# Optimization experiments

Hardware: AMD Instinct MI355X
Metric: run time of the kernel (lower is better)

## Reference

```python
import jax, jax.numpy as jnp
import numpy as np

N = 65536      # total nodes = B * MAXN
E = 524288     # edges (avg degree 8)
DX = 32; DG = 32
IN_DIM = DX + 3 * DG   # 128, after concat(x, g0, g1, g2)
H = 256; OUT = 8; MAXN = 8192


def setup_inputs() -> dict:
    key = jax.random.key(0)
    ks = jax.random.split(key, 40)
    inp = {}
    inp['x'] = jax.random.normal(ks[0], (N, DX), jnp.float32)
    inp['g0'] = jax.random.normal(ks[1], (N, DG), jnp.float32)
    inp['g1'] = jax.random.normal(ks[2], (N, DG), jnp.float32)
    inp['g2'] = jax.random.normal(ks[3], (N, DG), jnp.float32)
    inp['edge_src'] = jax.random.randint(ks[4], (E,), 0, N, jnp.int32)
    inp['edge_dst'] = jax.random.randint(ks[5], (E,), 0, N, jnp.int32)
    dims = [(IN_DIM, H), (H, H), (H, H), (H, H)]
    k = 6
    for i, (di, do) in enumerate(dims):
        s = 1.0 / np.sqrt(di)
        inp[f'Wl{i}'] = jax.random.uniform(ks[k], (di, do), jnp.float32, -s, s); k += 1
        inp[f'Wr{i}'] = jax.random.uniform(ks[k], (di, do), jnp.float32, -s, s); k += 1
        inp[f'b{i}'] = jnp.zeros((do,), jnp.float32)
    s = 1.0 / np.sqrt(MAXN)
    inp['mlp1_W1'] = jax.random.uniform(ks[k], (MAXN, H), jnp.float32, -s, s); k += 1
    inp['mlp1_b1'] = jnp.zeros((H,), jnp.float32)
    s = 1.0 / np.sqrt(H)
    inp['mlp1_W2'] = jax.random.uniform(ks[k], (H, 1), jnp.float32, -s, s); k += 1
    inp['mlp1_b2'] = jnp.zeros((1,), jnp.float32)
    inp['bn_gamma'] = jnp.ones((H,), jnp.float32)
    inp['bn_beta'] = jnp.zeros((H,), jnp.float32)
    inp['mlp2_W1'] = jax.random.uniform(ks[k], (H, H), jnp.float32, -s, s); k += 1
    inp['mlp2_b1'] = jnp.zeros((H,), jnp.float32)
    inp['mlp2_W2'] = jax.random.uniform(ks[k], (H, OUT), jnp.float32, -s, s); k += 1
    inp['mlp2_b2'] = jnp.zeros((OUT,), jnp.float32)
    return inp


def _forward(x, g0, g1, g2, edge_src, edge_dst,
             Wl0, Wr0, b0, Wl1, Wr1, b1, Wl2, Wr2, b2, Wl3, Wr3, b3,
             mlp1_W1, mlp1_b1, mlp1_W2, mlp1_b2, bn_gamma, bn_beta,
             mlp2_W1, mlp2_b1, mlp2_W2, mlp2_b2):
    h = jnp.concatenate([x, g0, g1, g2], axis=1)  # [N, IN_DIM]
    # mean-aggregation denominator (in-degree, clamped at 1 like PyG mean)
    cnt = jnp.maximum(
        jax.ops.segment_sum(jnp.ones((E,), h.dtype), edge_dst, num_segments=N), 1.0)
    for Wl, Wr, b in ((Wl0, Wr0, b0), (Wl1, Wr1, b1), (Wl2, Wr2, b2), (Wl3, Wr3, b3)):
        agg = jax.ops.segment_sum(h[edge_src], edge_dst, num_segments=N) / cnt[:, None]
        # SAGEConv: lin_l(mean of neighbors) + lin_r(self) + bias, then ReLU
        h = jax.nn.relu(agg @ Wl + h @ Wr + b)
        # F.dropout in eval / deterministic reference: identity
    h = h.reshape(-1, H, MAXN)                               # [B, H, MAXN]
    h = jax.nn.relu(jnp.einsum('bhm,mk->bhk', h, mlp1_W1) + mlp1_b1)
    h = (jnp.einsum('bhk,ko->bho', h, mlp1_W2) + mlp1_b2)[..., 0]  # [B, H]
    mean = h.mean(axis=0)
    var = h.var(axis=0)
    h = (h - mean) / jnp.sqrt(var + 1e-5) * bn_gamma + bn_beta
    h = jax.nn.relu(h)
    h = jax.nn.relu(h @ mlp2_W1 + mlp2_b1)
    return h @ mlp2_W2 + mlp2_b2                              # [B, OUT]


def reference(x, g0, g1, g2, edge_src, edge_dst,
              Wl0, Wr0, b0, Wl1, Wr1, b1, Wl2, Wr2, b2, Wl3, Wr3, b3,
              mlp1_W1, mlp1_b1, mlp1_W2, mlp1_b2, bn_gamma, bn_beta,
              mlp2_W1, mlp2_b1, mlp2_W2, mlp2_b2):
    return _forward(x, g0, g1, g2, edge_src, edge_dst,
                    Wl0, Wr0, b0, Wl1, Wr1, b1, Wl2, Wr2, b2, Wl3, Wr3, b3,
                    mlp1_W1, mlp1_b1, mlp1_W2, mlp1_b2, bn_gamma, bn_beta,
                    mlp2_W1, mlp2_b1, mlp2_W2, mlp2_b2)
```

## Files before the change

kernel.cpp:

```cpp
#include <hip/hip_runtime.h>
#include <hip/hip_bf16.h>


#define NN 65536
#define EE 524288
#define ROWS 65537
#define PCSR_CAP 983056

using frag16 = __attribute__((ext_vector_type(8))) short;
using f32x4  = __attribute__((ext_vector_type(4))) float;

__device__ __forceinline__ float b2f(unsigned short u) {
    union { unsigned u32; float f; } x; x.u32 = (unsigned)u << 16; return x.f;
}

__device__ __forceinline__ unsigned short f2b(float f) {
    return (unsigned short)(__bfloat16_as_ushort(__float2bfloat16(f)));
}

__device__ __forceinline__ void gld_lds16(const void* g, void* l) {
    __builtin_amdgcn_global_load_lds(
        (const __attribute__((address_space(1))) void*)g,
        (__attribute__((address_space(3))) void*)l, 16, 0, 0);
}


__global__ void gs_zero_deg(int* deg) {
    int i = blockIdx.x * 256 + threadIdx.x;
    if (i < NN) deg[i] = 0;
}

__global__ void gs_hist(const int* __restrict__ dst, int* __restrict__ deg) {
    int e = blockIdx.x * 256 + threadIdx.x;
    atomicAdd(&deg[dst[e]], 1);
}

__global__ void gs_deg_reduce(const int* __restrict__ deg, int* __restrict__ bsum) {
    int t = threadIdx.x;
    int p = (deg[blockIdx.x * 256 + t] + 7) & ~7;
#pragma unroll
    for (int off = 32; off > 0; off >>= 1) p += __shfl_down(p, off);
    __shared__ int w4[4];
    if ((t & 63) == 0) w4[t >> 6] = p;
    __syncthreads();
    if (t == 0) bsum[blockIdx.x] = w4[0] + w4[1] + w4[2] + w4[3];
}

__global__ void gs_scan_bsum(const int* __restrict__ bsum, int* __restrict__ bofs,
                             int* __restrict__ prow) {
    __shared__ int part[256];
    int t = threadIdx.x;
    int v = bsum[t];
    part[t] = v;
    __syncthreads();
    for (int off = 1; off < 256; off <<= 1) {
        int add = (t >= off) ? part[t - off] : 0;
        __syncthreads();
        part[t] += add;
        __syncthreads();
    }
    bofs[t] = part[t] - v;
    if (t == 255) prow[NN] = part[255];
}

__global__ void gs_scan_apply(const int* __restrict__ deg, const int* __restrict__ bofs,
                              int* __restrict__ prow, int* __restrict__ cursor,
                              float* __restrict__ inv_cnt, int* __restrict__ pcsr,
                              __hip_bfloat16* __restrict__ P0,
                              __hip_bfloat16* __restrict__ P1) {
    __shared__ int part[256];
    int t = threadIdx.x;
    int i = blockIdx.x * 256 + t;
    int d = deg[i];
    int p = (d + 7) & ~7;
    part[t] = p;
    __syncthreads();
    for (int off = 1; off < 256; off <<= 1) {
        int add = (t >= off) ? part[t - off] : 0;
        __syncthreads();
        part[t] += add;
        __syncthreads();
    }
    int beg = bofs[blockIdx.x] + part[t] - p;
    prow[i] = beg;
    cursor[i] = beg;
    inv_cnt[i] = 1.0f / (float)(d > 0 ? d : 1);
    for (int j = d; j < p; ++j) pcsr[beg + j] = NN;
    if (blockIdx.x == 0) {
        ((unsigned*)(P0 + (size_t)NN * 512))[t] = 0u;
        ((unsigned*)(P1 + (size_t)NN * 512))[t] = 0u;
        if (t < 16) pcsr[PCSR_CAP - 16 + t] = NN;
    }
}

__global__ void gs_bucket(const int* __restrict__ src, const int* __restrict__ dst,
                          int* __restrict__ cursor, int* __restrict__ pcsr) {
    int e = blockIdx.x * 256 + threadIdx.x;
    int d = dst[e];
    int p = atomicAdd(&cursor[d], 1);
    pcsr[p] = src[e];
}

struct TcvtArgs {
    const float* src[8];
    __hip_bfloat16* dst[8];
    int ldk[8];
    int kofs[8];
    int kblk[8];
};

__global__ void gs_tcvt_all(TcvtArgs a) {
    int z = blockIdx.z;
    if ((int)blockIdx.x >= a.kblk[z]) return;
    const float* src = a.src[z];
    __hip_bfloat16* dst = a.dst[z];
    int ldk = a.ldk[z], kofs = a.kofs[z];
    __shared__ float tile[32][33];
    int kb = blockIdx.x * 32, nb = blockIdx.y * 32;
    int tx = threadIdx.x, ty = threadIdx.y;
#pragma unroll
    for (int i = 0; i < 32; i += 8)
        tile[ty + i][tx] = src[(size_t)(kb + ty + i) * 256 + nb + tx];
    __syncthreads();
#pragma unroll
    for (int i = 0; i < 32; i += 8) {
        int n = nb + ty + i, k = kb + tx;
        dst[(size_t)n * ldk + kofs + k] = __float2bfloat16(tile[tx][ty + i]);
    }
}

__global__ void gs_tcvt(const float* __restrict__ src, __hip_bfloat16* __restrict__ dst,
                        int ldk, int kofs) {
    __shared__ float tile[32][33];
    int kb = blockIdx.x * 32, nb = blockIdx.y * 32;
    int tx = threadIdx.x, ty = threadIdx.y;
#pragma unroll
    for (int i = 0; i < 32; i += 8)
        tile[ty + i][tx] = src[(size_t)(kb + ty + i) * 256 + nb + tx];
    __syncthreads();
#pragma unroll
    for (int i = 0; i < 32; i += 8) {
        int n = nb + ty + i, k = kb + tx;
        dst[(size_t)n * ldk + kofs + k] = __float2bfloat16(tile[tx][ty + i]);
    }
}

__global__ void gs_concat_bf(const float* __restrict__ x, const float* __restrict__ g0,
                             const float* __restrict__ g1, const float* __restrict__ g2,
                             __hip_bfloat16* __restrict__ h) {
    int idx = blockIdx.x * 256 + threadIdx.x;
    int n = idx >> 7, c = idx & 127;
    float v;
    if (c < 32)       v = x[n * 32 + c];
    else if (c < 64)  v = g0[n * 32 + (c - 32)];
    else if (c < 96)  v = g1[n * 32 + (c - 64)];
    else              v = g2[n * 32 + (c - 96)];
    h[(size_t)n * 512 + 256 + c] = __float2bfloat16(v);
}

template <int DIM>
__global__ void gs_agg_bf(const __hip_bfloat16* __restrict__ hsrc,
                          __hip_bfloat16* __restrict__ adst,
                          const int* __restrict__ prow, const int* __restrict__ pcsr,
                          const float* __restrict__ inv_cnt) {
    int wave = threadIdx.x >> 6;
    int lane = threadIdx.x & 63;
    int n = blockIdx.x * 4 + wave;
    int e = prow[n], pe = prow[n + 1];
    float iv = inv_cnt[n];
    if constexpr (DIM == 256) {
        const __hip_bfloat16* base = hsrc + lane * 4;
        float a0 = 0.f, a1 = 0.f, a2 = 0.f, a3 = 0.f;
        int4 ia = *(const int4*)(pcsr + e);
        int4 ib = *(const int4*)(pcsr + e + 4);
        while (e < pe) {
            int4 c0 = ia, c1 = ib;
            e += 8;
            ia = *(const int4*)(pcsr + e);
            ib = *(const int4*)(pcsr + e + 4);
            ushort4 v0 = *(const ushort4*)(base + (size_t)c0.x * 512);
            ushort4 v1 = *(const ushort4*)(base + (size_t)c0.y * 512);
            ushort4 v2 = *(const ushort4*)(base + (size_t)c0.z * 512);
            ushort4 v3 = *(const ushort4*)(base + (size_t)c0.w * 512);
            ushort4 v4 = *(const ushort4*)(base + (size_t)c1.x * 512);
            ushort4 v5 = *(const ushort4*)(base + (size_t)c1.y * 512);
            ushort4 v6 = *(const ushort4*)(base + (size_t)c1.z * 512);
            ushort4 v7 = *(const ushort4*)(base + (size_t)c1.w * 512);
            a0 += b2f(v0.x); a1 += b2f(v0.y); a2 += b2f(v0.z); a3 += b2f(v0.w);
            a0 += b2f(v1.x); a1 += b2f(v1.y); a2 += b2f(v1.z); a3 += b2f(v1.w);
            a0 += b2f(v2.x); a1 += b2f(v2.y); a2 += b2f(v2.z); a3 += b2f(v2.w);
            a0 += b2f(v3.x); a1 += b2f(v3.y); a2 += b2f(v3.z); a3 += b2f(v3.w);
            a0 += b2f(v4.x); a1 += b2f(v4.y); a2 += b2f(v4.z); a3 += b2f(v4.w);
            a0 += b2f(v5.x); a1 += b2f(v5.y); a2 += b2f(v5.z); a3 += b2f(v5.w);
            a0 += b2f(v6.x); a1 += b2f(v6.y); a2 += b2f(v6.z); a3 += b2f(v6.w);
            a0 += b2f(v7.x); a1 += b2f(v7.y); a2 += b2f(v7.z); a3 += b2f(v7.w);
        }
        __hip_bfloat16 o[4] = {__float2bfloat16(a0 * iv), __float2bfloat16(a1 * iv),
                               __float2bfloat16(a2 * iv), __float2bfloat16(a3 * iv)};
        *(ushort4*)(adst + (size_t)n * 512 + lane * 4) = *(const ushort4*)o;
    } else {
        const __hip_bfloat16* base = hsrc + lane * 2;
        float a0 = 0.f, a1 = 0.f;
        int4 ia = *(const int4*)(pcsr + e);
        int4 ib = *(const int4*)(pcsr + e + 4);
        while (e < pe) {
            int4 c0 = ia, c1 = ib;
            e += 8;
            ia = *(const int4*)(pcsr + e);
            ib = *(const int4*)(pcsr + e + 4);
            ushort2 v0 = *(const ushort2*)(base + (size_t)c0.x * 512);
            ushort2 v1 = *(const ushort2*)(base + (size_t)c0.y * 512);
            ushort2 v2 = *(const ushort2*)(base + (size_t)c0.z * 512);
            ushort2 v3 = *(const ushort2*)(base + (size_t)c0.w * 512);
            ushort2 v4 = *(const ushort2*)(base + (size_t)c1.x * 512);
            ushort2 v5 = *(const ushort2*)(base + (size_t)c1.y * 512);
            ushort2 v6 = *(const ushort2*)(base + (size_t)c1.z * 512);
            ushort2 v7 = *(const ushort2*)(base + (size_t)c1.w * 512);
            a0 += b2f(v0.x); a1 += b2f(v0.y);
            a0 += b2f(v1.x); a1 += b2f(v1.y);
            a0 += b2f(v2.x); a1 += b2f(v2.y);
            a0 += b2f(v3.x); a1 += b2f(v3.y);
            a0 += b2f(v4.x); a1 += b2f(v4.y);
            a0 += b2f(v5.x); a1 += b2f(v5.y);
            a0 += b2f(v6.x); a1 += b2f(v6.y);
            a0 += b2f(v7.x); a1 += b2f(v7.y);
        }
        __hip_bfloat16 o[2] = {__float2bfloat16(a0 * iv), __float2bfloat16(a1 * iv)};
        *(ushort2*)(adst + (size_t)n * 512 + lane * 2) = *(const ushort2*)o;
    }
}

__device__ __forceinline__ void mfma_block_n256(const __hip_bfloat16* A, int lda,
                                                const __hip_bfloat16* Bt, int ldb,
                                                int kbeg, int kend, size_t row0,
                                                __hip_bfloat16* As, __hip_bfloat16* Bs,
                                                f32x4 acc[4][8]) {
    const int t = threadIdx.x;
    const int lane = t & 63;
    const int w = t >> 6;
    const int wr = (w >> 1) * 64;
    const int wc = (w & 1) * 128;
    const int sr8 = lane >> 3;
    const int scol = (lane & 7) * 8;
    for (int kc = kbeg; kc < kend; kc += 64) {
#pragma unroll
        for (int l = 0; l < 4; ++l)
            gld_lds16(A + (row0 + w * 32 + 8 * l + sr8) * (size_t)lda + kc + scol,
                      As + (w * 32 + 8 * l) * 64);
#pragma unroll
        for (int l = 0; l < 8; ++l)
            gld_lds16(Bt + (size_t)(w * 64 + 8 * l + sr8) * ldb + kc + scol,
                      Bs + (w * 64 + 8 * l) * 64);
        __syncthreads();
#pragma unroll
        for (int kk = 0; kk < 64; kk += 32) {
            frag16 af[4];
#pragma unroll
            for (int i = 0; i < 4; ++i)
                af[i] = *(const frag16*)(As + (wr + i * 16 + (lane & 15)) * 64 + kk + (lane >> 4) * 8);
#pragma unroll
            for (int j = 0; j < 8; ++j) {
                frag16 bf = *(const frag16*)(Bs + (wc + j * 16 + (lane & 15)) * 64 + kk + (lane >> 4) * 8);
#pragma unroll
                for (int i = 0; i < 4; ++i)
                    acc[i][j] = __builtin_amdgcn_mfma_f32_16x16x32_bf16(bf, af[i], acc[i][j], 0, 0, 0);
            }
        }
        __syncthreads();
    }
}

__global__ __launch_bounds__(256, 2)
void gs_gemm_bias_relu(const __hip_bfloat16* __restrict__ A, int lda, int K,
                       const __hip_bfloat16* __restrict__ Bt, int ldb,
                       const float* __restrict__ bias,
                       __hip_bfloat16* __restrict__ C, int ldc, int cofs) {
    __shared__ __hip_bfloat16 As[128 * 64];
    __shared__ __hip_bfloat16 Bs[256 * 64];
    f32x4 acc[4][8] = {};
    const size_t row0 = (size_t)blockIdx.x * 128;
    mfma_block_n256(A, lda, Bt, ldb, 0, K, row0, As, Bs, acc);
    const int lane = threadIdx.x & 63;
    const int w = threadIdx.x >> 6;
    const int wr = (w >> 1) * 64, wc = (w & 1) * 128;
#pragma unroll
    for (int j = 0; j < 8; ++j) {
        int nb = wc + j * 16 + (lane >> 4) * 4;
        const float4 bv = *(const float4*)&bias[nb];
#pragma unroll
        for (int i = 0; i < 4; ++i) {
            int m = wr + i * 16 + (lane & 15);
            unsigned short o[4];
            o[0] = f2b(fmaxf(acc[i][j][0] + bv.x, 0.f));
            o[1] = f2b(fmaxf(acc[i][j][1] + bv.y, 0.f));
            o[2] = f2b(fmaxf(acc[i][j][2] + bv.z, 0.f));
            o[3] = f2b(fmaxf(acc[i][j][3] + bv.w, 0.f));
            *(ushort4*)(C + (row0 + m) * (size_t)ldc + cofs + nb) = *(const ushort4*)o;
        }
    }
}

__global__ __launch_bounds__(256, 2)
void gs_gemm_splitk(const __hip_bfloat16* __restrict__ A, int lda,
                    const __hip_bfloat16* __restrict__ Bt, int ldb,
                    float* __restrict__ part) {
    __shared__ __hip_bfloat16 As[128 * 64];
    __shared__ __hip_bfloat16 Bs[256 * 64];
    f32x4 acc[4][8] = {};
    const size_t row0 = (size_t)blockIdx.x * 128;
    const int kbeg = blockIdx.y * 512;
    mfma_block_n256(A, lda, Bt, ldb, kbeg, kbeg + 512, row0, As, Bs, acc);
    const int lane = threadIdx.x & 63;
    const int w = threadIdx.x >> 6;
    const int wr = (w >> 1) * 64, wc = (w & 1) * 128;
    float* p = part + (size_t)blockIdx.y * 2048 * 256;
#pragma unroll
    for (int j = 0; j < 8; ++j) {
        int nb = wc + j * 16 + (lane >> 4) * 4;
#pragma unroll
        for (int i = 0; i < 4; ++i) {
            int m = wr + i * 16 + (lane & 15);
            *(f32x4*)(p + (row0 + m) * 256 + nb) = acc[i][j];
        }
    }
}

__global__ void gs_mlp1_reduce_pool(const float* __restrict__ part,
                                    const float* __restrict__ b1,
                                    const float* __restrict__ W2,
                                    const float* __restrict__ b2,
                                    float* __restrict__ pooled) {
    __shared__ float w4[4];
    int r = blockIdx.x;
    int t = threadIdx.x;
    size_t idx = (size_t)r * 256 + t;
    float s = 0.f;
#pragma unroll
    for (int ks = 0; ks < 16; ++ks) s += part[(size_t)ks * 524288 + idx];
    s = fmaxf(s + b1[t], 0.f) * W2[t];
#pragma unroll
    for (int off = 32; off > 0; off >>= 1) s += __shfl_down(s, off);
    if ((t & 63) == 0) w4[t >> 6] = s;
    __syncthreads();
    if (t == 0) pooled[r] = w4[0] + w4[1] + w4[2] + w4[3] + b2[0];
}

__global__ void gs_bn_mlp2(const float* __restrict__ pooled, const float* __restrict__ gamma,
                           const float* __restrict__ beta, const float* __restrict__ W1,
                           const float* __restrict__ b1, const float* __restrict__ W2,
                           const float* __restrict__ b2, float* __restrict__ out) {
    __shared__ float hb[8][256];
    __shared__ float h2[8][256];
    int t = threadIdx.x;
    {
        float v[8];
        float m = 0.f;
#pragma unroll
        for (int b = 0; b < 8; ++b) { v[b] = pooled[b * 256 + t]; m += v[b]; }
        m *= 0.125f;
        float var = 0.f;
#pragma unroll
        for (int b = 0; b < 8; ++b) { float d = v[b] - m; var += d * d; }
        var *= 0.125f;
        float is = 1.0f / sqrtf(var + 1e-5f);
        float g = gamma[t], bt = beta[t];
#pragma unroll
        for (int b = 0; b < 8; ++b) hb[b][t] = fmaxf((v[b] - m) * is * g + bt, 0.f);
    }
    __syncthreads();
    {
        float acc[8] = {};
        for (int i = 0; i < 256; ++i) {
            float w = W1[i * 256 + t];
#pragma unroll
            for (int b = 0; b < 8; ++b) acc[b] = fmaf(hb[b][i], w, acc[b]);
        }
        float bb = b1[t];
#pragma unroll
        for (int b = 0; b < 8; ++b) h2[b][t] = fmaxf(acc[b] + bb, 0.f);
    }
    __syncthreads();
    if (t < 64) {
        int b = t >> 3, o = t & 7;
        float acc = 0.f;
        for (int j = 0; j < 256; ++j) acc = fmaf(h2[b][j], W2[j * 8 + o], acc);
        out[b * 8 + o] = acc + b2[o];
    }
}

extern "C" void kernel_launch(void* const* d_in, const int* in_sizes, int n_in,
                              void* d_out, int out_size, void* d_ws, size_t ws_size,
                              hipStream_t stream) {
    const float* x  = (const float*)d_in[0];
    const float* g0 = (const float*)d_in[1];
    const float* g1 = (const float*)d_in[2];
    const float* g2 = (const float*)d_in[3];
    const int* edge_src = (const int*)d_in[4];
    const int* edge_dst = (const int*)d_in[5];
    const float* Wl[4] = {(const float*)d_in[6], (const float*)d_in[9],
                          (const float*)d_in[12], (const float*)d_in[15]};
    const float* Wr[4] = {(const float*)d_in[7], (const float*)d_in[10],
                          (const float*)d_in[13], (const float*)d_in[16]};
    const float* bs[4] = {(const float*)d_in[8], (const float*)d_in[11],
                          (const float*)d_in[14], (const float*)d_in[17]};
    const float* mlp1_W1 = (const float*)d_in[18];
    const float* mlp1_b1 = (const float*)d_in[19];
    const float* mlp1_W2 = (const float*)d_in[20];
    const float* mlp1_b2 = (const float*)d_in[21];
    const float* bn_gamma = (const float*)d_in[22];
    const float* bn_beta  = (const float*)d_in[23];
    const float* mlp2_W1 = (const float*)d_in[24];
    const float* mlp2_b1 = (const float*)d_in[25];
    const float* mlp2_W2 = (const float*)d_in[26];
    const float* mlp2_b2 = (const float*)d_in[27];
    float* out = (float*)d_out;

    char* ws = (char*)d_ws;
    __hip_bfloat16* P0 = (__hip_bfloat16*)ws;
    __hip_bfloat16* P1 = P0 + (size_t)ROWS * 512;
    __hip_bfloat16* WC0 = P1 + (size_t)ROWS * 512;
    __hip_bfloat16* WC1 = WC0 + 65536;
    __hip_bfloat16* WC2 = WC1 + 131072;
    __hip_bfloat16* WC3 = WC2 + 131072;
    __hip_bfloat16* W1T = WC3 + 131072;
    float* inv_cnt = (float*)(W1T + 2097152);
    int* ideg = (int*)(inv_cnt + 65536);
    int* prow = ideg + 65536;
    int* cursor = prow + 65544;
    int* bsum = cursor + 65536;
    int* bofs = bsum + 256;
    int* pcsr = bofs + 256;
    __hip_bfloat16* H4 = P0;
    float* pooled = (float*)((char*)P1 + (size_t)(2 << 20));
    float* PART = (float*)((char*)P1 + (size_t)(4 << 20));

    gs_zero_deg<<<256, 256, 0, stream>>>(ideg);
    gs_hist<<<EE / 256, 256, 0, stream>>>(edge_dst, ideg);
    gs_deg_reduce<<<256, 256, 0, stream>>>(ideg, bsum);
    gs_scan_bsum<<<1, 256, 0, stream>>>(bsum, bofs, prow);
    gs_scan_apply<<<256, 256, 0, stream>>>(ideg, bofs, prow, cursor, inv_cnt, pcsr, P0, P1);
    gs_bucket<<<EE / 256, 256, 0, stream>>>(edge_src, edge_dst, cursor, pcsr);

    {
        TcvtArgs a;
        const float* srcs[8] = {Wl[0], Wr[0], Wl[1], Wr[1], Wl[2], Wr[2], Wl[3], Wr[3]};
        __hip_bfloat16* dsts[8] = {WC0, WC0, WC1, WC1, WC2, WC2, WC3, WC3};
        int ldks[8] = {256, 256, 512, 512, 512, 512, 512, 512};
        int kofss[8] = {0, 128, 0, 256, 0, 256, 0, 256};
        int kblks[8] = {4, 4, 8, 8, 8, 8, 8, 8};
        for (int i = 0; i < 8; ++i) {
            a.src[i] = srcs[i]; a.dst[i] = dsts[i];
            a.ldk[i] = ldks[i]; a.kofs[i] = kofss[i]; a.kblk[i] = kblks[i];
        }
        gs_tcvt_all<<<dim3(8, 8, 8), dim3(32, 8), 0, stream>>>(a);
    }
    gs_tcvt<<<dim3(256, 8), dim3(32, 8), 0, stream>>>(mlp1_W1, W1T, 8192, 0);

    gs_concat_bf<<<NN * 128 / 256, 256, 0, stream>>>(x, g0, g1, g2, P0);

    gs_agg_bf<128><<<NN / 4, 256, 0, stream>>>(P0 + 256, P0 + 128, prow, pcsr, inv_cnt);
    gs_gemm_bias_relu<<<NN / 128, 256, 0, stream>>>(P0 + 128, 512, 256, WC0, 256,
                                                    bs[0], P1, 512, 256);
    gs_agg_bf<256><<<NN / 4, 256, 0, stream>>>(P1 + 256, P1, prow, pcsr, inv_cnt);
    gs_gemm_bias_relu<<<NN / 128, 256, 0, stream>>>(P1, 512, 512, WC1, 512,
                                                    bs[1], P0, 512, 256);
    gs_agg_bf<256><<<NN / 4, 256, 0, stream>>>(P0 + 256, P0, prow, pcsr, inv_cnt);
    gs_gemm_bias_relu<<<NN / 128, 256, 0, stream>>>(P0, 512, 512, WC2, 512,
                                                    bs[2], P1, 512, 256);
    gs_agg_bf<256><<<NN / 4, 256, 0, stream>>>(P1 + 256, P1, prow, pcsr, inv_cnt);
    gs_gemm_bias_relu<<<NN / 128, 256, 0, stream>>>(P1, 512, 512, WC3, 512,
                                                    bs[3], H4, 256, 0);

    gs_gemm_splitk<<<dim3(16, 16), 256, 0, stream>>>(H4, 8192, W1T, 8192, PART);
    gs_mlp1_reduce_pool<<<2048, 256, 0, stream>>>(PART, mlp1_b1, mlp1_W2, mlp1_b2, pooled);

    gs_bn_mlp2<<<1, 256, 0, stream>>>(pooled, bn_gamma, bn_beta, mlp2_W1, mlp2_b1,
                                      mlp2_W2, mlp2_b2, out);
}
```

Baseline: 531.1 us.

## Fuse neighbor mean-aggregation into SAGE GEMM via LDS-staged aggregate tiles

```diff
diff --git a/kernel.cpp b/kernel.cpp
--- a/kernel.cpp
+++ b/kernel.cpp
@@ -158,75 +158,138 @@
     h[(size_t)n * 512 + 256 + c] = __float2bfloat16(v);
 }
 
-template <int DIM>
-__global__ void gs_agg_bf(const __hip_bfloat16* __restrict__ hsrc,
-                          __hip_bfloat16* __restrict__ adst,
-                          const int* __restrict__ prow, const int* __restrict__ pcsr,
-                          const float* __restrict__ inv_cnt) {
-    int wave = threadIdx.x >> 6;
-    int lane = threadIdx.x & 63;
-    int n = blockIdx.x * 4 + wave;
-    int e = prow[n], pe = prow[n + 1];
-    float iv = inv_cnt[n];
-    if constexpr (DIM == 256) {
-        const __hip_bfloat16* base = hsrc + lane * 4;
-        float a0 = 0.f, a1 = 0.f, a2 = 0.f, a3 = 0.f;
-        int4 ia = *(const int4*)(pcsr + e);
-        int4 ib = *(const int4*)(pcsr + e + 4);
-        while (e < pe) {
-            int4 c0 = ia, c1 = ib;
-            e += 8;
-            ia = *(const int4*)(pcsr + e);
-            ib = *(const int4*)(pcsr + e + 4);
-            ushort4 v0 = *(const ushort4*)(base + (size_t)c0.x * 512);
-            ushort4 v1 = *(const ushort4*)(base + (size_t)c0.y * 512);
-            ushort4 v2 = *(const ushort4*)(base + (size_t)c0.z * 512);
-            ushort4 v3 = *(const ushort4*)(base + (size_t)c0.w * 512);
-            ushort4 v4 = *(const ushort4*)(base + (size_t)c1.x * 512);
-            ushort4 v5 = *(const ushort4*)(base + (size_t)c1.y * 512);
-            ushort4 v6 = *(const ushort4*)(base + (size_t)c1.z * 512);
-            ushort4 v7 = *(const ushort4*)(base + (size_t)c1.w * 512);
-            a0 += b2f(v0.x); a1 += b2f(v0.y); a2 += b2f(v0.z); a3 += b2f(v0.w);
-            a0 += b2f(v1.x); a1 += b2f(v1.y); a2 += b2f(v1.z); a3 += b2f(v1.w);
-            a0 += b2f(v2.x); a1 += b2f(v2.y); a2 += b2f(v2.z); a3 += b2f(v2.w);
-            a0 += b2f(v3.x); a1 += b2f(v3.y); a2 += b2f(v3.z); a3 += b2f(v3.w);
-            a0 += b2f(v4.x); a1 += b2f(v4.y); a2 += b2f(v4.z); a3 += b2f(v4.w);
-            a0 += b2f(v5.x); a1 += b2f(v5.y); a2 += b2f(v5.z); a3 += b2f(v5.w);
-            a0 += b2f(v6.x); a1 += b2f(v6.y); a2 += b2f(v6.z); a3 += b2f(v6.w);
-            a0 += b2f(v7.x); a1 += b2f(v7.y); a2 += b2f(v7.z); a3 += b2f(v7.w);
-        }
-        __hip_bfloat16 o[4] = {__float2bfloat16(a0 * iv), __float2bfloat16(a1 * iv),
-                               __float2bfloat16(a2 * iv), __float2bfloat16(a3 * iv)};
-        *(ushort4*)(adst + (size_t)n * 512 + lane * 4) = *(const ushort4*)o;
-    } else {
-        const __hip_bfloat16* base = hsrc + lane * 2;
-        float a0 = 0.f, a1 = 0.f;
-        int4 ia = *(const int4*)(pcsr + e);
-        int4 ib = *(const int4*)(pcsr + e + 4);
-        while (e < pe) {
-            int4 c0 = ia, c1 = ib;
-            e += 8;
-            ia = *(const int4*)(pcsr + e);
-            ib = *(const int4*)(pcsr + e + 4);
-            ushort2 v0 = *(const ushort2*)(base + (size_t)c0.x * 512);
-            ushort2 v1 = *(const ushort2*)(base + (size_t)c0.y * 512);
-            ushort2 v2 = *(const ushort2*)(base + (size_t)c0.z * 512);
-            ushort2 v3 = *(const ushort2*)(base + (size_t)c0.w * 512);
-            ushort2 v4 = *(const ushort2*)(base + (size_t)c1.x * 512);
-            ushort2 v5 = *(const ushort2*)(base + (size_t)c1.y * 512);
-            ushort2 v6 = *(const ushort2*)(base + (size_t)c1.z * 512);
-            ushort2 v7 = *(const ushort2*)(base + (size_t)c1.w * 512);
-            a0 += b2f(v0.x); a1 += b2f(v0.y);
-            a0 += b2f(v1.x); a1 += b2f(v1.y);
-            a0 += b2f(v2.x); a1 += b2f(v2.y);
-            a0 += b2f(v3.x); a1 += b2f(v3.y);
-            a0 += b2f(v4.x); a1 += b2f(v4.y);
-            a0 += b2f(v5.x); a1 += b2f(v5.y);
-            a0 += b2f(v6.x); a1 += b2f(v6.y);
-            a0 += b2f(v7.x); a1 += b2f(v7.y);
-        }
-        __hip_bfloat16 o[2] = {__float2bfloat16(a0 * iv), __float2bfloat16(a1 * iv)};
-        *(ushort2*)(adst + (size_t)n * 512 + lane * 2) = *(const ushort2*)o;
+template <int AGGK, int HK>
+__global__ __launch_bounds__(256, 2)
+void gs_sage_fused(const __hip_bfloat16* __restrict__ hsrc,
+                   const int* __restrict__ prow, const int* __restrict__ pcsr,
+                   const float* __restrict__ inv_cnt,
+                   const __hip_bfloat16* __restrict__ Bt, int ldb,
+                   const float* __restrict__ bias,
+                   __hip_bfloat16* __restrict__ C, int ldc, int cofs) {
+    __shared__ char smem[65536];
+    __hip_bfloat16* AggS = (__hip_bfloat16*)smem;
+    __hip_bfloat16* As   = (__hip_bfloat16*)smem;
+    __hip_bfloat16* Bs   = (__hip_bfloat16*)(smem + 32768);
+    const int t = threadIdx.x;
+    const int lane = t & 63;
+    const int w = t >> 6;
+    const size_t row0 = (size_t)blockIdx.x * 128;
+    const int wr = (w >> 1) * 64, wc = (w & 1) * 128;
+    const int sr8 = lane >> 3, scol = (lane & 7) * 8;
+    f32x4 acc[4][8] = {};
+
+    int pv = 0; float ivv = 0.f;
+    {
+        int base = (int)row0 + w * 32;
+        if (lane <= 32) pv = prow[base + lane];
+        if (lane < 32) ivv = inv_cnt[base + lane];
+    }
+
+    for (int c = 0; c < AGGK; c += 128) {
+        for (int i = 0; i < 32; ++i) {
+            int e = __shfl(pv, i);
+            int pe = __shfl(pv, i + 1);
+            float iv = __shfl(ivv, i);
+            const __hip_bfloat16* gbase = hsrc + c + lane * 2;
+            float a0 = 0.f, a1 = 0.f;
+            int4 ia = *(const int4*)(pcsr + e);
+            int4 ib = *(const int4*)(pcsr + e + 4);
+            while (e < pe) {
+                int4 c0 = ia, c1 = ib;
+                e += 8;
+                ia = *(const int4*)(pcsr + e);
+                ib = *(const int4*)(pcsr + e + 4);
+                ushort2 v0 = *(const ushort2*)(gbase + (size_t)c0.x * 512);
+                ushort2 v1 = *(const ushort2*)(gbase + (size_t)c0.y * 512);
+                ushort2 v2 = *(const ushort2*)(gbase + (size_t)c0.z * 512);
+                ushort2 v3 = *(const ushort2*)(gbase + (size_t)c0.w * 512);
+                ushort2 v4 = *(const ushort2*)(gbase + (size_t)c1.x * 512);
+                ushort2 v5 = *(const ushort2*)(gbase + (size_t)c1.y * 512);
+                ushort2 v6 = *(const ushort2*)(gbase + (size_t)c1.z * 512);
+                ushort2 v7 = *(const ushort2*)(gbase + (size_t)c1.w * 512);
+                a0 += b2f(v0.x); a1 += b2f(v0.y);
+                a0 += b2f(v1.x); a1 += b2f(v1.y);
+                a0 += b2f(v2.x); a1 += b2f(v2.y);
+                a0 += b2f(v3.x); a1 += b2f(v3.y);
+                a0 += b2f(v4.x); a1 += b2f(v4.y);
+                a0 += b2f(v5.x); a1 += b2f(v5.y);
+                a0 += b2f(v6.x); a1 += b2f(v6.y);
+                a0 += b2f(v7.x); a1 += b2f(v7.y);
+            }
+            unsigned short o0 = f2b(a0 * iv), o1 = f2b(a1 * iv);
+            ushort2 ov; ov.x = o0; ov.y = o1;
+            *(ushort2*)(AggS + (w * 32 + i) * 128 + lane * 2) = ov;
+        }
+        __syncthreads();
+        for (int kc2 = 0; kc2 < 128; kc2 += 64) {
+#pragma unroll
+            for (int l = 0; l < 8; ++l)
+                gld_lds16(Bt + (size_t)(w * 64 + 8 * l + sr8) * ldb + c + kc2 + scol,
+                          Bs + (w * 64 + 8 * l) * 64);
+            __syncthreads();
+#pragma unroll
+            for (int kk = 0; kk < 64; kk += 32) {
+                frag16 af[4];
+#pragma unroll
+                for (int i2 = 0; i2 < 4; ++i2)
+                    af[i2] = *(const frag16*)(AggS + (wr + i2 * 16 + (lane & 15)) * 128
+                                              + kc2 + kk + (lane >> 4) * 8);
+#pragma unroll
+                for (int j = 0; j < 8; ++j) {
+                    frag16 bf = *(const frag16*)(Bs + (wc + j * 16 + (lane & 15)) * 64
+                                                 + kk + (lane >> 4) * 8);
+#pragma unroll
+                    for (int i2 = 0; i2 < 4; ++i2)
+                        acc[i2][j] = __builtin_amdgcn_mfma_f32_16x16x32_bf16(
+                            bf, af[i2], acc[i2][j], 0, 0, 0);
+                }
+            }
+            __syncthreads();
+        }
+    }
+    for (int kc = 0; kc < HK; kc += 64) {
+#pragma unroll
+        for (int l = 0; l < 4; ++l)
+            gld_lds16(hsrc + (row0 + w * 32 + 8 * l + sr8) * 512 + kc + scol,
+                      As + (w * 32 + 8 * l) * 64);
+#pragma unroll
+        for (int l = 0; l < 8; ++l)
+            gld_lds16(Bt + (size_t)(w * 64 + 8 * l + sr8) * ldb + AGGK + kc + scol,
+                      Bs + (w * 64 + 8 * l) * 64);
+        __syncthreads();
+#pragma unroll
+        for (int kk = 0; kk < 64; kk += 32) {
+            frag16 af[4];
+#pragma unroll
+            for (int i2 = 0; i2 < 4; ++i2)
+                af[i2] = *(const frag16*)(As + (wr + i2 * 16 + (lane & 15)) * 64
+                                          + kk + (lane >> 4) * 8);
+#pragma unroll
+            for (int j = 0; j < 8; ++j) {
+                frag16 bf = *(const frag16*)(Bs + (wc + j * 16 + (lane & 15)) * 64
+                                             + kk + (lane >> 4) * 8);
+#pragma unroll
+                for (int i2 = 0; i2 < 4; ++i2)
+                    acc[i2][j] = __builtin_amdgcn_mfma_f32_16x16x32_bf16(
+                        bf, af[i2], acc[i2][j], 0, 0, 0);
+            }
+        }
+        __syncthreads();
+    }
+#pragma unroll
+    for (int j = 0; j < 8; ++j) {
+        int nb = wc + j * 16 + (lane >> 4) * 4;
+        const float4 bv = *(const float4*)&bias[nb];
+#pragma unroll
+        for (int i = 0; i < 4; ++i) {
+            int m = wr + i * 16 + (lane & 15);
+            unsigned short o[4];
+            o[0] = f2b(fmaxf(acc[i][j][0] + bv.x, 0.f));
+            o[1] = f2b(fmaxf(acc[i][j][1] + bv.y, 0.f));
+            o[2] = f2b(fmaxf(acc[i][j][2] + bv.z, 0.f));
+            o[3] = f2b(fmaxf(acc[i][j][3] + bv.w, 0.f));
+            *(ushort4*)(C + (row0 + m) * (size_t)ldc + cofs + nb) = *(const ushort4*)o;
+        }
     }
 }
 
@@ -267,36 +330,6 @@
             }
         }
         __syncthreads();
-    }
-}
-
-__global__ __launch_bounds__(256, 2)
-void gs_gemm_bias_relu(const __hip_bfloat16* __restrict__ A, int lda, int K,
-                       const __hip_bfloat16* __restrict__ Bt, int ldb,
-                       const float* __restrict__ bias,
-                       __hip_bfloat16* __restrict__ C, int ldc, int cofs) {
-    __shared__ __hip_bfloat16 As[128 * 64];
-    __shared__ __hip_bfloat16 Bs[256 * 64];
-    f32x4 acc[4][8] = {};
-    const size_t row0 = (size_t)blockIdx.x * 128;
-    mfma_block_n256(A, lda, Bt, ldb, 0, K, row0, As, Bs, acc);
-    const int lane = threadIdx.x & 63;
-    const int w = threadIdx.x >> 6;
-    const int wr = (w >> 1) * 64, wc = (w & 1) * 128;
-#pragma unroll
-    for (int j = 0; j < 8; ++j) {
-        int nb = wc + j * 16 + (lane >> 4) * 4;
-        const float4 bv = *(const float4*)&bias[nb];
-#pragma unroll
-        for (int i = 0; i < 4; ++i) {
-            int m = wr + i * 16 + (lane & 15);
-            unsigned short o[4];
-            o[0] = f2b(fmaxf(acc[i][j][0] + bv.x, 0.f));
-            o[1] = f2b(fmaxf(acc[i][j][1] + bv.y, 0.f));
-            o[2] = f2b(fmaxf(acc[i][j][2] + bv.z, 0.f));
-            o[3] = f2b(fmaxf(acc[i][j][3] + bv.w, 0.f));
-            *(ushort4*)(C + (row0 + m) * (size_t)ldc + cofs + nb) = *(const ushort4*)o;
-        }
     }
 }
 
@@ -458,18 +491,14 @@
 
     gs_concat_bf<<<NN * 128 / 256, 256, 0, stream>>>(x, g0, g1, g2, P0);
 
-    gs_agg_bf<128><<<NN / 4, 256, 0, stream>>>(P0 + 256, P0 + 128, prow, pcsr, inv_cnt);
-    gs_gemm_bias_relu<<<NN / 128, 256, 0, stream>>>(P0 + 128, 512, 256, WC0, 256,
-                                                    bs[0], P1, 512, 256);
-    gs_agg_bf<256><<<NN / 4, 256, 0, stream>>>(P1 + 256, P1, prow, pcsr, inv_cnt);
-    gs_gemm_bias_relu<<<NN / 128, 256, 0, stream>>>(P1, 512, 512, WC1, 512,
-                                                    bs[1], P0, 512, 256);
-    gs_agg_bf<256><<<NN / 4, 256, 0, stream>>>(P0 + 256, P0, prow, pcsr, inv_cnt);
-    gs_gemm_bias_relu<<<NN / 128, 256, 0, stream>>>(P0, 512, 512, WC2, 512,
-                                                    bs[2], P1, 512, 256);
-    gs_agg_bf<256><<<NN / 4, 256, 0, stream>>>(P1 + 256, P1, prow, pcsr, inv_cnt);
-    gs_gemm_bias_relu<<<NN / 128, 256, 0, stream>>>(P1, 512, 512, WC3, 512,
-                                                    bs[3], H4, 256, 0);
+    gs_sage_fused<128, 128><<<NN / 128, 256, 0, stream>>>(
+        P0 + 256, prow, pcsr, inv_cnt, WC0, 256, bs[0], P1, 512, 256);
+    gs_sage_fused<256, 256><<<NN / 128, 256, 0, stream>>>(
+        P1 + 256, prow, pcsr, inv_cnt, WC1, 512, bs[1], P0, 512, 256);
+    gs_sage_fused<256, 256><<<NN / 128, 256, 0, stream>>>(
+        P0 + 256, prow, pcsr, inv_cnt, WC2, 512, bs[2], P1, 512, 256);
+    gs_sage_fused<256, 256><<<NN / 128, 256, 0, stream>>>(
+        P1 + 256, prow, pcsr, inv_cnt, WC3, 512, bs[3], H4, 256, 0);
 
     gs_gemm_splitk<<<dim3(16, 16), 256, 0, stream>>>(H4, 8192, W1T, 8192, PART);
     gs_mlp1_reduce_pool<<<2048, 256, 0, stream>>>(PART, mlp1_b1, mlp1_W2, mlp1_b2, pooled);
```

Result: slower. 672.1 us (+26.5%).
